# Kernel optimization log

Measured on AMD Instinct MI355X. Metric: run time of the kernel, lower is better.

## Reference

```python
import jax, jax.numpy as jnp
import numpy as np

EPS_NORM = 1e-6
EPS_MM = 1e-5


def feature_l2norm(f, axis=1):
    # torch: f / sqrt(sum(f^2, dim) + 1e-6)
    return f / jnp.sqrt(jnp.sum(f * f, axis=axis, keepdims=True) + EPS_NORM)


def mutual_matching(c):
    # c: [b, 1, f1, f2, f3, f4]
    b, ch, f1, f2, f3, f4 = c.shape
    # max over (f1,f2) for each (f3,f4) target location
    max_B = jnp.max(c.reshape(b, f1 * f2, f3, f4), axis=1).reshape(b, 1, 1, 1, f3, f4)
    # max over (f3,f4) for each (f1,f2) source location
    max_A = jnp.max(c.reshape(b, f1 * f2, f3 * f4), axis=2).reshape(b, 1, f1, f2, 1, 1)
    return c * (c / (max_A + EPS_MM)) * (c / (max_B + EPS_MM))


def correlation4d(fa, fb):
    # fa: [b,c,hA,wA], fb: [b,c,hB,wB] -> [b,1,hA,wA,hB,wB]
    corr = jnp.einsum('bcij,bckl->bijkl', fa, fb)[:, None]
    corr = jax.nn.relu(corr)
    return feature_l2norm(corr, axis=1)  # channel dim is 1 -> x/sqrt(x^2+eps)


def conv4d(x, w, b):
    # x: [B,Ci,f1,f2,f3,f4]; w: [Co,Ci,k,k,k,k]; b: [Co]
    # Implemented as a sum of k 3D convs over (f2,f3,f4), sliding along f1 --
    # exactly the Conv4d emulation used by NC-Net.
    B, Ci, f1, f2, f3, f4 = x.shape
    Co, _, k = w.shape[:3]
    p = k // 2
    xp = jnp.pad(x, ((0, 0), (0, 0), (p, p), (0, 0), (0, 0), (0, 0)))
    out = None
    for i in range(k):
        xi = jax.lax.dynamic_slice_in_dim(xp, i, f1, axis=2)        # [B,Ci,f1,f2,f3,f4]
        xi = xi.transpose(0, 2, 1, 3, 4, 5).reshape(B * f1, Ci, f2, f3, f4)
        yi = jax.lax.conv_general_dilated(
            xi, w[:, :, i], window_strides=(1, 1, 1),
            padding=[(p, p)] * 3,
            dimension_numbers=('NCDHW', 'OIDHW', 'NCDHW'))
        yi = yi.reshape(B, f1, Co, f2, f3, f4).transpose(0, 2, 1, 3, 4, 5)
        out = yi if out is None else out + yi
    return out + b[None, :, None, None, None, None]


def nc_stack(x, params):
    # Sequential(Conv4d, ReLU) x 3
    for w, b in params:
        x = jax.nn.relu(conv4d(x, w, b))
    return x


def neigh_consensus(x, params):
    # symmetric mode: conv(x) + conv(x.permute(0,1,4,5,2,3)).permute back
    ya = nc_stack(x, params)
    yb = nc_stack(x.transpose(0, 1, 4, 5, 2, 3), params).transpose(0, 1, 4, 5, 2, 3)
    return ya + yb


def setup_inputs() -> dict:
    key = jax.random.key(0)
    ks = jax.random.split(key, 8)
    b, c, h, w = 4, 256, 32, 32
    feature_A = jax.random.normal(ks[0], (b, c, h, w), dtype=jnp.float32)
    feature_B = jax.random.normal(ks[1], (b, c, h, w), dtype=jnp.float32)
    k = 3
    w1 = jax.random.normal(ks[2], (10, 1, k, k, k, k), dtype=jnp.float32) * 0.05
    b1 = jnp.zeros((10,), jnp.float32)
    w2 = jax.random.normal(ks[3], (10, 10, k, k, k, k), dtype=jnp.float32) * 0.05
    b2 = jnp.zeros((10,), jnp.float32)
    w3 = jax.random.normal(ks[4], (1, 10, k, k, k, k), dtype=jnp.float32) * 0.05
    b3 = jnp.zeros((1,), jnp.float32)
    return {"feature_A": feature_A, "feature_B": feature_B,
            "w1": w1, "b1": b1, "w2": w2, "b2": b2, "w3": w3, "b3": b3}


def reference(feature_A, feature_B, w1, b1, w2, b2, w3, b3):
    fa = feature_l2norm(feature_A, axis=1)
    fb = feature_l2norm(feature_B, axis=1)
    corr4d = correlation4d(fa, fb)                   # [b,1,hA,wA,hB,wB]
    corr4d = mutual_matching(corr4d)
    corr4d = neigh_consensus(corr4d, [(w1, b1), (w2, b2), (w3, b3)])
    corr4d = mutual_matching(corr4d)
    return corr4d
```

## Files before the change

kernel.cpp:

```cpp
#include <hip/hip_runtime.h>

#define EPSN 1e-6f
#define EPSM 1e-5f

typedef __fp16 h2v __attribute__((ext_vector_type(2)));

__device__ __forceinline__ unsigned pkh2(float a, float b) {
    union { h2v h; unsigned u; } v;
    v.h = __builtin_amdgcn_cvt_pkrtz(a, b);
    return v.u;
}

__device__ __forceinline__ float dot2f(unsigned a, unsigned b, float c) {
    union { unsigned u; h2v h; } ua, ub;
    ua.u = a; ub.u = b;
#if __has_builtin(__builtin_amdgcn_fdot2)
    return __builtin_amdgcn_fdot2(ua.h, ub.h, c, false);
#else
    return fmaf((float)ua.h.x, (float)ub.h.x,
                fmaf((float)ua.h.y, (float)ub.h.y, c));
#endif
}

__global__ __launch_bounds__(256) void invnorm_k(const float* __restrict__ f,
                                                 float* __restrict__ inv)
{
    int pbase = blockIdx.x * 64;
    int pp = threadIdx.x & 63;
    int cc = threadIdx.x >> 6;
    int pos = pbase + pp;
    int b = pos >> 10, ij = pos & 1023;
    const float* fp = f + (size_t)(b * 256) * 1024 + ij;
    float s = 0.f;
    #pragma unroll 8
    for (int k = 0; k < 64; ++k) {
        float v = fp[(size_t)(cc * 64 + k) * 1024];
        s += v * v;
    }
    __shared__ float red[4][64];
    red[cc][pp] = s;
    __syncthreads();
    if (cc == 0) {
        float t = red[0][pp] + red[1][pp] + red[2][pp] + red[3][pp];
        inv[pos] = rsqrtf(t + EPSN);
    }
}

__global__ __launch_bounds__(256) void corr_k(const float* __restrict__ fa,
                                              const float* __restrict__ fb,
                                              const float* __restrict__ invA,
                                              const float* __restrict__ invB,
                                              float* __restrict__ corr)
{
    __shared__ float As[16][68];
    __shared__ float Bs[16][68];
    int b = blockIdx.z;
    int i0 = blockIdx.y * 64, j0 = blockIdx.x * 64;
    int tid = threadIdx.x;
    int tx = tid & 15, ty = tid >> 4;
    const float* fab = fa + (size_t)b * 256 * 1024;
    const float* fbb = fb + (size_t)b * 256 * 1024;
    const float* ia = invA + b * 1024 + i0;
    const float* ib = invB + b * 1024 + j0;
    float acc[4][4] = {};
    for (int kc = 0; kc < 256; kc += 16) {
        #pragma unroll
        for (int l = 0; l < 4; ++l) {
            int idx = tid + l * 256;
            int r = idx >> 6, cix = idx & 63;
            As[r][cix] = fab[(size_t)(kc + r) * 1024 + i0 + cix] * ia[cix];
            Bs[r][cix] = fbb[(size_t)(kc + r) * 1024 + j0 + cix] * ib[cix];
        }
        __syncthreads();
        #pragma unroll
        for (int k = 0; k < 16; ++k) {
            float4 av = *(const float4*)&As[k][ty * 4];
            float4 bv = *(const float4*)&Bs[k][tx * 4];
            float a[4] = {av.x, av.y, av.z, av.w};
            float bq[4] = {bv.x, bv.y, bv.z, bv.w};
            #pragma unroll
            for (int ii = 0; ii < 4; ++ii)
                #pragma unroll
                for (int jj = 0; jj < 4; ++jj)
                    acc[ii][jj] += a[ii] * bq[jj];
        }
        __syncthreads();
    }
    float* cb = corr + ((size_t)b << 20);
    #pragma unroll
    for (int ii = 0; ii < 4; ++ii) {
        float4 o; float v;
        v = fmaxf(acc[ii][0], 0.f); o.x = v * rsqrtf(v * v + EPSN);
        v = fmaxf(acc[ii][1], 0.f); o.y = v * rsqrtf(v * v + EPSN);
        v = fmaxf(acc[ii][2], 0.f); o.z = v * rsqrtf(v * v + EPSN);
        v = fmaxf(acc[ii][3], 0.f); o.w = v * rsqrtf(v * v + EPSN);
        *(float4*)&cb[(size_t)(i0 + ty * 4 + ii) * 1024 + j0 + tx * 4] = o;
    }
}

__global__ __launch_bounds__(256) void rowmax_k(const float* __restrict__ c,
                                                float* __restrict__ maxR)
{
    int b = blockIdx.y, i = blockIdx.x, tid = threadIdx.x;
    const float* row = c + ((size_t)b << 20) + ((size_t)i << 10);
    float m = fmaxf(fmaxf(row[tid], row[tid + 256]), fmaxf(row[tid + 512], row[tid + 768]));
    #pragma unroll
    for (int off = 32; off; off >>= 1) m = fmaxf(m, __shfl_down(m, off, 64));
    __shared__ float sred[4];
    if ((tid & 63) == 0) sred[tid >> 6] = m;
    __syncthreads();
    if (tid == 0)
        maxR[b * 1024 + i] = fmaxf(fmaxf(sred[0], sred[1]), fmaxf(sred[2], sred[3]));
}

__global__ __launch_bounds__(256) void colmax_k(const float* __restrict__ c,
                                                float* __restrict__ maxC)
{
    int j = blockIdx.x * 256 + threadIdx.x;
    int r0 = blockIdx.y * 128;
    int b = blockIdx.z;
    const float* cb = c + ((size_t)b << 20);
    float m = 0.f;
    for (int r = 0; r < 128; ++r) m = fmaxf(m, cb[(size_t)(r0 + r) * 1024 + j]);
    atomicMax((int*)&maxC[b * 1024 + j], __float_as_int(m));
}

__global__ __launch_bounds__(256) void mmapply_k(float* __restrict__ c,
                                                 const float* __restrict__ maxR,
                                                 const float* __restrict__ maxC)
{
    int e4 = blockIdx.x * 256 + threadIdx.x;
    int e = e4 * 4;
    int b = e >> 20, i = (e >> 10) & 1023, j0 = e & 1023;
    float4 v = ((float4*)c)[e4];
    float ra = 1.f / (maxR[b * 1024 + i] + EPSM);
    float4 mb = ((const float4*)maxC)[(b * 1024 + j0) >> 2];
    float4 o;
    o.x = v.x * v.x * v.x * ra / (mb.x + EPSM);
    o.y = v.y * v.y * v.y * ra / (mb.y + EPSM);
    o.z = v.z * v.z * v.z * ra / (mb.z + EPSM);
    o.w = v.w * v.w * v.w * ra / (mb.w + EPSM);
    ((float4*)c)[e4] = o;
}

template <int CI, int CO>
__global__ void packw_k(const float* __restrict__ w, float* __restrict__ dst, int perm)
{
    constexpr int WS = (3 * CO + 3) & ~3;
    int idx = blockIdx.x * 256 + threadIdx.x;
    if (idx >= CI * 27 * WS) return;
    int ci = idx / (27 * WS);
    int rem = idx - ci * 27 * WS;
    int d123 = rem / WS;
    int slot = rem - d123 * WS;
    float v = 0.f;
    if (slot < 3 * CO) {
        int d4 = slot / CO, co = slot - d4 * CO;
        int t = d123 * 3 + d4;
        int d1 = t / 27, r2 = t % 27;
        int d2 = r2 / 9, r3 = r2 % 9;
        int d3 = r3 / 3, dd4 = r3 % 3;
        int st = perm ? (d3 * 27 + dd4 * 9 + d1 * 3 + d2) : t;
        v = w[(co * CI + ci) * 81 + st];
    }
    dst[idx] = v;
}

template <int CIP, int CO>
__global__ void packw2_k(const float* __restrict__ w, unsigned* __restrict__ dst, int perm)
{
    constexpr int WS = (3 * CO + 3) & ~3;
    int idx = blockIdx.x * 256 + threadIdx.x;
    if (idx >= CIP * 27 * WS) return;
    int pp = idx / (27 * WS);
    int rem = idx - pp * 27 * WS;
    int d123 = rem / WS;
    int slot = rem - d123 * WS;
    unsigned v = 0u;
    if (slot < 3 * CO) {
        int d4 = slot / CO, co = slot - d4 * CO;
        int t = d123 * 3 + d4;
        int d1 = t / 27, r2 = t % 27;
        int d2 = r2 / 9, r3 = r2 % 9;
        int d3 = r3 / 3, dd4 = r3 % 3;
        int st = perm ? (d3 * 27 + dd4 * 9 + d1 * 3 + d2) : t;
        float f0 = w[(co * 2 * CIP + 2 * pp) * 81 + st];
        float f1 = w[(co * 2 * CIP + 2 * pp + 1) * 81 + st];
        v = pkh2(f0, f1);
    }
    dst[idx] = v;
}

template <int CI, int CO, bool ADD>
__global__ __launch_bounds__(256, 4) void conv4d_k(const float* __restrict__ x,
                                                   const float* __restrict__ wp,
                                                   const float* __restrict__ bias,
                                                   float* __restrict__ y)
{
    constexpr int WS = (3 * CO + 3) & ~3;
    constexpr int NW4 = WS / 4;
    constexpr int SLAB = 34 * 35;
    __shared__ float tile[3 * SLAB];

    int tid = threadIdx.x;
    int f1 = blockIdx.x >> 5, f2 = blockIdx.x & 31;
    int q = tid & 7, yy = tid >> 3;
    int x0 = q << 2;

    for (int e = tid; e < 3 * SLAB; e += 256) tile[e] = 0.f;

    float acc[CO][4];
    #pragma unroll
    for (int co = 0; co < CO; ++co) {
        float bv = bias[co];
        acc[co][0] = bv; acc[co][1] = bv; acc[co][2] = bv; acc[co][3] = bv;
    }

    float bufA[WS], bufB[WS];

#define TAP(U, WB, WN, PF) do {                                               \
        constexpr int u_ = (U);                                               \
        const float* rowb_ = &tile[(u_/3)*SLAB + (yy + u_%3)*35 + x0];        \
        float xs_[6];                                                         \
        _Pragma("unroll") for (int j = 0; j < 6; ++j) xs_[j] = rowb_[j];      \
        if (PF) {                                                             \
            _Pragma("unroll") for (int k = 0; k < NW4; ++k)                   \
                *(float4*)&WN[k*4] =                                          \
                    ((const float4*)(wphase + (u_+1)*WS))[k];                 \
        }                                                                     \
        _Pragma("unroll") for (int d4 = 0; d4 < 3; ++d4)                      \
        _Pragma("unroll") for (int co = 0; co < CO; ++co) {                   \
            float wf_ = WB[d4*CO + co];                                       \
            _Pragma("unroll") for (int p = 0; p < 4; ++p)                     \
                acc[co][p] = fmaf(xs_[p + d4], wf_, acc[co][p]);              \
        }                                                                     \
    } while (0)

    #pragma unroll 1
    for (int ci = 0; ci < CI; ++ci) {
        const float* wci = wp + ci * 27 * WS;
        #pragma unroll 1
        for (int d1 = 0; d1 < 3; ++d1) {
            int g1 = f1 + d1 - 1;
            bool g1ok = (unsigned)g1 < 32u;
            const float* wphase = wci + d1 * 9 * WS;
            __syncthreads();
            #pragma unroll
            for (int k = 0; k < NW4; ++k)
                *(float4*)&bufA[k*4] = ((const float4*)wphase)[k];
            #pragma unroll
            for (int it = 0; it < 3; ++it) {
                int e = tid + it * 256;
                int s2 = e >> 8, rr = (e >> 3) & 31, qq = e & 7;
                int g2 = f2 + s2 - 1;
                float4 v = {0.f, 0.f, 0.f, 0.f};
                if (g1ok & ((unsigned)g2 < 32u))
                    v = *(const float4*)&x[((size_t)ci << 20) +
                        ((size_t)((g1 << 5) + g2) << 10) + (rr << 5) + (qq << 2)];
                float* t = &tile[s2 * SLAB + (rr + 1) * 35 + 1 + (qq << 2)];
                t[0] = v.x; t[1] = v.y; t[2] = v.z; t[3] = v.w;
            }
            __syncthreads();

            TAP(0, bufA, bufB, true);
            TAP(1, bufB, bufA, true);
            TAP(2, bufA, bufB, true);
            TAP(3, bufB, bufA, true);
            TAP(4, bufA, bufB, true);
            TAP(5, bufB, bufA, true);
            TAP(6, bufA, bufB, true);
            TAP(7, bufB, bufA, true);
            TAP(8, bufA, bufB, false);
        }
    }
#undef TAP

    size_t obase = ((size_t)(f1 * 32 + f2) << 10) + yy * 32 + x0;
    #pragma unroll
    for (int co = 0; co < CO; ++co) {
        float4 o;
        o.x = fmaxf(acc[co][0], 0.f);
        o.y = fmaxf(acc[co][1], 0.f);
        o.z = fmaxf(acc[co][2], 0.f);
        o.w = fmaxf(acc[co][3], 0.f);
        float* yp = y + ((size_t)co << 20) + obase;
        if (ADD) {
            float4 prev = *(const float4*)yp;
            o.x += prev.x; o.y += prev.y; o.z += prev.z; o.w += prev.w;
        }
        *(float4*)yp = o;
    }
}

template <int CIP, int CO, bool ADD>
__global__ __launch_bounds__(256, 4) void conv4dp_k(const float* __restrict__ x,
                                                    const unsigned* __restrict__ wp,
                                                    const float* __restrict__ bias,
                                                    float* __restrict__ y)
{
    constexpr int WS = (3 * CO + 3) & ~3;
    constexpr int NW4 = WS / 4;
    constexpr int SLAB = 34 * 35;
    __shared__ unsigned tile[3 * SLAB];

    int tid = threadIdx.x;
    int f1 = blockIdx.x >> 5, f2 = blockIdx.x & 31;
    int q = tid & 7, yy = tid >> 3;
    int x0 = q << 2;

    for (int e = tid; e < 3 * SLAB; e += 256) tile[e] = 0u;

    float acc[CO][4];
    #pragma unroll
    for (int co = 0; co < CO; ++co) {
        float bv = bias[co];
        acc[co][0] = bv; acc[co][1] = bv; acc[co][2] = bv; acc[co][3] = bv;
    }

    unsigned bufA[WS], bufB[WS];

#define TAPP(U, WB, WN, PF) do {                                              \
        constexpr int u_ = (U);                                               \
        const unsigned* rowb_ = &tile[(u_/3)*SLAB + (yy + u_%3)*35 + x0];     \
        unsigned xs_[6];                                                      \
        _Pragma("unroll") for (int j = 0; j < 6; ++j) xs_[j] = rowb_[j];      \
        if (PF) {                                                             \
            _Pragma("unroll") for (int k = 0; k < NW4; ++k)                   \
                *(uint4*)&WN[k*4] =                                           \
                    ((const uint4*)(wphase + (u_+1)*WS))[k];                  \
        }                                                                     \
        _Pragma("unroll") for (int d4 = 0; d4 < 3; ++d4)                      \
        _Pragma("unroll") for (int co = 0; co < CO; ++co) {                   \
            unsigned wf_ = WB[d4*CO + co];                                    \
            _Pragma("unroll") for (int p = 0; p < 4; ++p)                     \
                acc[co][p] = dot2f(xs_[p + d4], wf_, acc[co][p]);             \
        }                                                                     \
    } while (0)

    #pragma unroll 1
    for (int pp = 0; pp < CIP; ++pp) {
        const float* xc0 = x + ((size_t)(2 * pp) << 20);
        const float* xc1 = x + ((size_t)(2 * pp + 1) << 20);
        const unsigned* wci = wp + pp * 27 * WS;
        #pragma unroll 1
        for (int d1 = 0; d1 < 3; ++d1) {
            int g1 = f1 + d1 - 1;
            bool g1ok = (unsigned)g1 < 32u;
            const unsigned* wphase = wci + d1 * 9 * WS;
            __syncthreads();
            #pragma unroll
            for (int k = 0; k < NW4; ++k)
                *(uint4*)&bufA[k*4] = ((const uint4*)wphase)[k];
            #pragma unroll
            for (int it = 0; it < 3; ++it) {
                int e = tid + it * 256;
                int s2 = e >> 8, rr = (e >> 3) & 31, qq = e & 7;
                int g2 = f2 + s2 - 1;
                float4 va = {0.f, 0.f, 0.f, 0.f};
                float4 vb = {0.f, 0.f, 0.f, 0.f};
                if (g1ok & ((unsigned)g2 < 32u)) {
                    size_t off = ((size_t)((g1 << 5) + g2) << 10) + (rr << 5) + (qq << 2);
                    va = *(const float4*)&xc0[off];
                    vb = *(const float4*)&xc1[off];
                }
                unsigned* t = &tile[s2 * SLAB + (rr + 1) * 35 + 1 + (qq << 2)];
                t[0] = pkh2(va.x, vb.x);
                t[1] = pkh2(va.y, vb.y);
                t[2] = pkh2(va.z, vb.z);
                t[3] = pkh2(va.w, vb.w);
            }
            __syncthreads();

            TAPP(0, bufA, bufB, true);
            TAPP(1, bufB, bufA, true);
            TAPP(2, bufA, bufB, true);
            TAPP(3, bufB, bufA, true);
            TAPP(4, bufA, bufB, true);
            TAPP(5, bufB, bufA, true);
            TAPP(6, bufA, bufB, true);
            TAPP(7, bufB, bufA, true);
            TAPP(8, bufA, bufB, false);
        }
    }
#undef TAPP

    size_t obase = ((size_t)(f1 * 32 + f2) << 10) + yy * 32 + x0;
    #pragma unroll
    for (int co = 0; co < CO; ++co) {
        float4 o;
        o.x = fmaxf(acc[co][0], 0.f);
        o.y = fmaxf(acc[co][1], 0.f);
        o.z = fmaxf(acc[co][2], 0.f);
        o.w = fmaxf(acc[co][3], 0.f);
        float* yp = y + ((size_t)co << 20) + obase;
        if (ADD) {
            float4 prev = *(const float4*)yp;
            o.x += prev.x; o.y += prev.y; o.z += prev.z; o.w += prev.w;
        }
        *(float4*)yp = o;
    }
}

extern "C" void kernel_launch(void* const* d_in, const int* in_sizes, int n_in,
                              void* d_out, int out_size, void* d_ws, size_t ws_size,
                              hipStream_t stream)
{
    (void)in_sizes; (void)n_in; (void)out_size; (void)ws_size;
    const float* fA = (const float*)d_in[0];
    const float* fB = (const float*)d_in[1];
    const float* w1 = (const float*)d_in[2];
    const float* b1 = (const float*)d_in[3];
    const float* w2 = (const float*)d_in[4];
    const float* b2 = (const float*)d_in[5];
    const float* w3 = (const float*)d_in[6];
    const float* b3 = (const float*)d_in[7];
    float* out = (float*)d_out;
    float* ws = (float*)d_ws;

    size_t o = 0;
    float* invA = ws + o; o += 4096;
    float* invB = ws + o; o += 4096;
    float* maxR = ws + o; o += 4096;
    float* maxC = ws + o; o += 4096;
    float* pw1  = ws + o; o += 2048;
    unsigned* pw2 = (unsigned*)(ws + o); o += 8640;
    unsigned* pw3 = (unsigned*)(ws + o); o += 1080;
    float* corr = ws + o; o += 4194304;
    float* t1   = ws + o; o += 10485760;
    float* t2   = ws + o; o += 10485760;

    invnorm_k<<<64, 256, 0, stream>>>(fA, invA);
    invnorm_k<<<64, 256, 0, stream>>>(fB, invB);
    corr_k<<<dim3(16, 16, 4), 256, 0, stream>>>(fA, fB, invA, invB, corr);

    rowmax_k<<<dim3(1024, 4), 256, 0, stream>>>(corr, maxR);
    (void)hipMemsetAsync(maxC, 0, 4096 * sizeof(float), stream);
    colmax_k<<<dim3(4, 8, 4), 256, 0, stream>>>(corr, maxC);
    mmapply_k<<<4096, 256, 0, stream>>>(corr, maxR, maxC);

    packw_k<1, 10><<<4, 256, 0, stream>>>(w1, pw1, 0);
    packw_k<1, 10><<<4, 256, 0, stream>>>(w1, pw1 + 864, 1);
    packw2_k<5, 10><<<17, 256, 0, stream>>>(w2, pw2, 0);
    packw2_k<5, 10><<<17, 256, 0, stream>>>(w2, pw2 + 4320, 1);
    packw2_k<5, 1><<<3, 256, 0, stream>>>(w3, pw3, 0);
    packw2_k<5, 1><<<3, 256, 0, stream>>>(w3, pw3 + 540, 1);

    for (int b = 0; b < 4; ++b) {
        const float* xb = corr + (size_t)b * 1048576;
        float* ob = out + (size_t)b * 1048576;
        conv4d_k<1, 10, false><<<1024, 256, 0, stream>>>(xb, pw1, b1, t1);
        conv4dp_k<5, 10, false><<<1024, 256, 0, stream>>>(t1, pw2, b2, t2);
        conv4dp_k<5, 1, false><<<1024, 256, 0, stream>>>(t2, pw3, b3, ob);
        conv4d_k<1, 10, false><<<1024, 256, 0, stream>>>(xb, pw1 + 864, b1, t1);
        conv4dp_k<5, 10, false><<<1024, 256, 0, stream>>>(t1, pw2 + 4320, b2, t2);
        conv4dp_k<5, 1, true ><<<1024, 256, 0, stream>>>(t2, pw3 + 540, b3, ob);
    }

    rowmax_k<<<dim3(1024, 4), 256, 0, stream>>>(out, maxR);
    (void)hipMemsetAsync(maxC, 0, 4096 * sizeof(float), stream);
    colmax_k<<<dim3(4, 8, 4), 256, 0, stream>>>(out, maxC);
    mmapply_k<<<4096, 256, 0, stream>>>(out, maxR, maxC);
}
```

Before: 1.829 ms.

## Use MFMA f16 for middle 10-to-10 conv4d and store intermediates as packed half

Replaces the middle 10x10-channel conv4d, previously done with packed fdot2 in VALU, with a new kernel that runs 16x16x16 f16 MFMA instructions over the 81 taps, keeping the input channels padded to 16 in a shared-memory tile. The first and middle layers now write their outputs as packed fp16 channel pairs, which halves intermediate memory traffic and lets later layers skip the float-to-half conversion on load. The cost is padding waste (10 of 16 channels used), many small scalar global loads when filling the tile, and additional fp16 rounding of the intermediate activations.

Result: faster. 1.659 ms (-9.3%).

```diff
diff --git a/kernel.cpp b/kernel.cpp
--- a/kernel.cpp
+++ b/kernel.cpp
@@ -4,6 +4,10 @@
 #define EPSM 1e-5f
 
 typedef __fp16 h2v __attribute__((ext_vector_type(2)));
+typedef __fp16 f16x4 __attribute__((ext_vector_type(4)));
+typedef float f32x4 __attribute__((ext_vector_type(4)));
+
+#define MFMA16(a, b, c) __builtin_amdgcn_mfma_f32_16x16x16f16((a), (b), (c), 0, 0, 0)
 
 __device__ __forceinline__ unsigned pkh2(float a, float b) {
     union { h2v h; unsigned u; } v;
@@ -164,6 +168,27 @@
         v = w[(co * CI + ci) * 81 + st];
     }
     dst[idx] = v;
+}
+
+__global__ void packwm_k(const float* __restrict__ w, unsigned short* __restrict__ dst,
+                         int perm)
+{
+    int idx = blockIdx.x * 256 + threadIdx.x;
+    if (idx >= 20736) return;
+    int tap = idx >> 8;
+    int co  = (idx >> 4) & 15;
+    int k   = idx & 15;
+    float v = 0.f;
+    if (co < 10 && k < 10) {
+        int d1 = tap / 27, r2 = tap % 27;
+        int d2 = r2 / 9, r3 = r2 % 9;
+        int d3 = r3 / 3, d4 = r3 % 3;
+        int st = perm ? (d3 * 27 + d4 * 9 + d1 * 3 + d2) : tap;
+        v = w[(co * 10 + k) * 81 + st];
+    }
+    union { __fp16 h; unsigned short u; } cv;
+    cv.h = (__fp16)v;
+    dst[idx] = cv.u;
 }
 
 template <int CIP, int CO>
@@ -191,7 +216,7 @@
     dst[idx] = v;
 }
 
-template <int CI, int CO, bool ADD>
+template <int CI, int CO, bool ADD, bool PACK>
 __global__ __launch_bounds__(256, 4) void conv4d_k(const float* __restrict__ x,
                                                    const float* __restrict__ wp,
                                                    const float* __restrict__ bias,
@@ -276,24 +301,146 @@
 #undef TAP
 
     size_t obase = ((size_t)(f1 * 32 + f2) << 10) + yy * 32 + x0;
+    if (PACK) {
+        unsigned* ypu = (unsigned*)y;
+        #pragma unroll
+        for (int c = 0; c < CO / 2; ++c) {
+            uint4 o;
+            o.x = pkh2(fmaxf(acc[2*c][0], 0.f), fmaxf(acc[2*c+1][0], 0.f));
+            o.y = pkh2(fmaxf(acc[2*c][1], 0.f), fmaxf(acc[2*c+1][1], 0.f));
+            o.z = pkh2(fmaxf(acc[2*c][2], 0.f), fmaxf(acc[2*c+1][2], 0.f));
+            o.w = pkh2(fmaxf(acc[2*c][3], 0.f), fmaxf(acc[2*c+1][3], 0.f));
+            *(uint4*)&ypu[(size_t)c * 1048576 + obase] = o;
+        }
+    } else {
+        #pragma unroll
+        for (int co = 0; co < CO; ++co) {
+            float4 o;
+            o.x = fmaxf(acc[co][0], 0.f);
+            o.y = fmaxf(acc[co][1], 0.f);
+            o.z = fmaxf(acc[co][2], 0.f);
+            o.w = fmaxf(acc[co][3], 0.f);
+            float* yp = y + ((size_t)co << 20) + obase;
+            if (ADD) {
+                float4 prev = *(const float4*)yp;
+                o.x += prev.x; o.y += prev.y; o.z += prev.z; o.w += prev.w;
+            }
+            *(float4*)yp = o;
+        }
+    }
+}
+
+__global__ __launch_bounds__(256, 4) void conv4dm_k(const unsigned* __restrict__ xp,
+                                                    const unsigned short* __restrict__ wm,
+                                                    const float* __restrict__ bias,
+                                                    unsigned* __restrict__ yp)
+{
+    __shared__ unsigned tile[3 * 10 * 34 * 9];
+
+    int tid = threadIdx.x;
+    int bx = blockIdx.x;
+    int q  = bx & 3;
+    int f2 = (bx >> 2) & 31;
+    int f1 = bx >> 7;
+    int l  = tid & 63;
+    int wv = tid >> 6;
+    int sl = l & 15;
+    int g  = l >> 4;
+
+    for (int e = tid; e < 9180; e += 256) tile[e] = 0u;
+
+    f32x4 bv;
     #pragma unroll
-    for (int co = 0; co < CO; ++co) {
-        float4 o;
-        o.x = fmaxf(acc[co][0], 0.f);
-        o.y = fmaxf(acc[co][1], 0.f);
-        o.z = fmaxf(acc[co][2], 0.f);
-        o.w = fmaxf(acc[co][3], 0.f);
-        float* yp = y + ((size_t)co << 20) + obase;
-        if (ADD) {
-            float4 prev = *(const float4*)yp;
-            o.x += prev.x; o.y += prev.y; o.z += prev.z; o.w += prev.w;
-        }
-        *(float4*)yp = o;
-    }
+    for (int e = 0; e < 4; ++e) {
+        int co = 4 * g + e;
+        bv[e] = (co < 10) ? bias[co] : 0.f;
+    }
+    f32x4 acc0 = bv, acc1 = bv, acc2 = bv, acc3 = bv;
+
+    int qbase = q * 8;
+
+    #pragma unroll 1
+    for (int d1 = 0; d1 < 3; ++d1) {
+        int g1 = f1 + d1 - 1;
+        bool g1ok = (unsigned)g1 < 32u;
+        __syncthreads();
+
+        uint2 aw[27];
+        #pragma unroll
+        for (int t27 = 0; t27 < 27; ++t27) {
+            int tap = d1 * 27 + t27;
+            aw[t27] = *(const uint2*)&wm[(tap << 8) + (sl << 4) + (g << 2)];
+        }
+
+        #pragma unroll
+        for (int it = 0; it < 4; ++it) {
+            int e = tid + it * 256;
+            if (e < 960) {
+                int c  = (e & 31) + 1;
+                int rg = e >> 5;
+                int r  = rg % 10;
+                int s2 = rg / 10;
+                int g2 = f2 + s2 - 1;
+                int g3 = qbase + r - 1;
+                unsigned v0 = 0, v1 = 0, v2 = 0, v3 = 0, v4 = 0;
+                if (g1ok & ((unsigned)g2 < 32u) & ((unsigned)g3 < 32u)) {
+                    size_t off = ((size_t)((g1 << 5) + g2) << 10) + (g3 << 5) + (c - 1);
+                    v0 = xp[off];
+                    v1 = xp[off + 1048576];
+                    v2 = xp[off + 2097152];
+                    v3 = xp[off + 3145728];
+                    v4 = xp[off + 4194304];
+                }
+                unsigned* t = &tile[((s2 * 10 + r) * 34 + c) * 9];
+                t[0] = v0; t[1] = v1; t[2] = v2; t[3] = v3; t[4] = v4;
+            }
+        }
+        __syncthreads();
+
+        int tb0 = ((wv * 2 + 0) * 34 + sl) * 9 + (g << 1);
+        #pragma unroll
+        for (int d2 = 0; d2 < 3; ++d2)
+        #pragma unroll
+        for (int d3 = 0; d3 < 3; ++d3)
+        #pragma unroll
+        for (int d4 = 0; d4 < 3; ++d4) {
+            int t27 = d2 * 9 + d3 * 3 + d4;
+            union { uint2 u; f16x4 h; } A; A.u = aw[t27];
+            int tapoff = ((d2 * 10 + d3) * 34 + d4) * 9;
+            const unsigned* bp = &tile[tb0 + tapoff];
+            union { uint2 u; f16x4 h; } B;
+            B.u.x = bp[0];           B.u.y = bp[1];
+            acc0 = MFMA16(A.h, B.h, acc0);
+            B.u.x = bp[16 * 9];      B.u.y = bp[16 * 9 + 1];
+            acc1 = MFMA16(A.h, B.h, acc1);
+            B.u.x = bp[34 * 9];      B.u.y = bp[34 * 9 + 1];
+            acc2 = MFMA16(A.h, B.h, acc2);
+            B.u.x = bp[50 * 9];      B.u.y = bp[50 * 9 + 1];
+            acc3 = MFMA16(A.h, B.h, acc3);
+        }
+    }
+
+    size_t pbase = ((size_t)((f1 << 5) + f2) << 10);
+#define STORE_TILE(ACC, RT, CH) do {                                          \
+        size_t sidx = pbase + ((size_t)(qbase + (RT)) << 5) + (CH) * 16 + sl; \
+        float r0 = fmaxf((ACC)[0], 0.f), r1 = fmaxf((ACC)[1], 0.f);           \
+        float r2 = fmaxf((ACC)[2], 0.f), r3 = fmaxf((ACC)[3], 0.f);           \
+        if (g < 2) {                                                          \
+            yp[(size_t)(2 * g)     * 1048576 + sidx] = pkh2(r0, r1);          \
+            yp[(size_t)(2 * g + 1) * 1048576 + sidx] = pkh2(r2, r3);          \
+        } else if (g == 2) {                                                  \
+            yp[(size_t)4 * 1048576 + sidx] = pkh2(r0, r1);                    \
+        }                                                                     \
+    } while (0)
+    STORE_TILE(acc0, wv * 2 + 0, 0);
+    STORE_TILE(acc1, wv * 2 + 0, 1);
+    STORE_TILE(acc2, wv * 2 + 1, 0);
+    STORE_TILE(acc3, wv * 2 + 1, 1);
+#undef STORE_TILE
 }
 
 template <int CIP, int CO, bool ADD>
-__global__ __launch_bounds__(256, 4) void conv4dp_k(const float* __restrict__ x,
+__global__ __launch_bounds__(256, 4) void conv4dp_k(const unsigned* __restrict__ xp,
                                                     const unsigned* __restrict__ wp,
                                                     const float* __restrict__ bias,
                                                     float* __restrict__ y)
@@ -313,8 +460,8 @@
     float acc[CO][4];
     #pragma unroll
     for (int co = 0; co < CO; ++co) {
-        float bv = bias[co];
-        acc[co][0] = bv; acc[co][1] = bv; acc[co][2] = bv; acc[co][3] = bv;
+        float bvv = bias[co];
+        acc[co][0] = bvv; acc[co][1] = bvv; acc[co][2] = bvv; acc[co][3] = bvv;
     }
 
     unsigned bufA[WS], bufB[WS];
@@ -339,8 +486,6 @@
 
     #pragma unroll 1
     for (int pp = 0; pp < CIP; ++pp) {
-        const float* xc0 = x + ((size_t)(2 * pp) << 20);
-        const float* xc1 = x + ((size_t)(2 * pp + 1) << 20);
         const unsigned* wci = wp + pp * 27 * WS;
         #pragma unroll 1
         for (int d1 = 0; d1 < 3; ++d1) {
@@ -356,18 +501,12 @@
                 int e = tid + it * 256;
                 int s2 = e >> 8, rr = (e >> 3) & 31, qq = e & 7;
                 int g2 = f2 + s2 - 1;
-                float4 va = {0.f, 0.f, 0.f, 0.f};
-                float4 vb = {0.f, 0.f, 0.f, 0.f};
-                if (g1ok & ((unsigned)g2 < 32u)) {
-                    size_t off = ((size_t)((g1 << 5) + g2) << 10) + (rr << 5) + (qq << 2);
-                    va = *(const float4*)&xc0[off];
-                    vb = *(const float4*)&xc1[off];
-                }
+                uint4 v = {0u, 0u, 0u, 0u};
+                if (g1ok & ((unsigned)g2 < 32u))
+                    v = *(const uint4*)&xp[((size_t)pp << 20) +
+                        ((size_t)((g1 << 5) + g2) << 10) + (rr << 5) + (qq << 2)];
                 unsigned* t = &tile[s2 * SLAB + (rr + 1) * 35 + 1 + (qq << 2)];
-                t[0] = pkh2(va.x, vb.x);
-                t[1] = pkh2(va.y, vb.y);
-                t[2] = pkh2(va.z, vb.z);
-                t[3] = pkh2(va.w, vb.w);
+                t[0] = v.x; t[1] = v.y; t[2] = v.z; t[3] = v.w;
             }
             __syncthreads();
 
@@ -392,12 +531,12 @@
         o.y = fmaxf(acc[co][1], 0.f);
         o.z = fmaxf(acc[co][2], 0.f);
         o.w = fmaxf(acc[co][3], 0.f);
-        float* yp = y + ((size_t)co << 20) + obase;
+        float* ypt = y + ((size_t)co << 20) + obase;
         if (ADD) {
-            float4 prev = *(const float4*)yp;
+            float4 prev = *(const float4*)ypt;
             o.x += prev.x; o.y += prev.y; o.z += prev.z; o.w += prev.w;
         }
-        *(float4*)yp = o;
+        *(float4*)ypt = o;
     }
 }
 
@@ -423,11 +562,11 @@
     float* maxR = ws + o; o += 4096;
     float* maxC = ws + o; o += 4096;
     float* pw1  = ws + o; o += 2048;
-    unsigned* pw2 = (unsigned*)(ws + o); o += 8640;
+    unsigned short* wm2 = (unsigned short*)(ws + o); o += 20736;
     unsigned* pw3 = (unsigned*)(ws + o); o += 1080;
     float* corr = ws + o; o += 4194304;
-    float* t1   = ws + o; o += 10485760;
-    float* t2   = ws + o; o += 10485760;
+    unsigned* t1p = (unsigned*)(ws + o); o += 5242880;
+    unsigned* t2p = (unsigned*)(ws + o); o += 5242880;
 
     invnorm_k<<<64, 256, 0, stream>>>(fA, invA);
     invnorm_k<<<64, 256, 0, stream>>>(fB, invB);
@@ -440,20 +579,20 @@
 
     packw_k<1, 10><<<4, 256, 0, stream>>>(w1, pw1, 0);
     packw_k<1, 10><<<4, 256, 0, stream>>>(w1, pw1 + 864, 1);
-    packw2_k<5, 10><<<17, 256, 0, stream>>>(w2, pw2, 0);
-    packw2_k<5, 10><<<17, 256, 0, stream>>>(w2, pw2 + 4320, 1);
+    packwm_k<<<81, 256, 0, stream>>>(w2, wm2, 0);
+    packwm_k<<<81, 256, 0, stream>>>(w2, wm2 + 20736, 1);
     packw2_k<5, 1><<<3, 256, 0, stream>>>(w3, pw3, 0);
     packw2_k<5, 1><<<3, 256, 0, stream>>>(w3, pw3 + 540, 1);
 
     for (int b = 0; b < 4; ++b) {
         const float* xb = corr + (size_t)b * 1048576;
         float* ob = out + (size_t)b * 1048576;
-        conv4d_k<1, 10, false><<<1024, 256, 0, stream>>>(xb, pw1, b1, t1);
-        conv4dp_k<5, 10, false><<<1024, 256, 0, stream>>>(t1, pw2, b2, t2);
-        conv4dp_k<5, 1, false><<<1024, 256, 0, stream>>>(t2, pw3, b3, ob);
-        conv4d_k<1, 10, false><<<1024, 256, 0, stream>>>(xb, pw1 + 864, b1, t1);
-        conv4dp_k<5, 10, false><<<1024, 256, 0, stream>>>(t1, pw2 + 4320, b2, t2);
-        conv4dp_k<5, 1, true ><<<1024, 256, 0, stream>>>(t2, pw3 + 540, b3, ob);
+        conv4d_k<1, 10, false, true><<<1024, 256, 0, stream>>>(xb, pw1, b1, (float*)t1p);
+        conv4dm_k<<<4096, 256, 0, stream>>>(t1p, wm2, b2, t2p);
+        conv4dp_k<5, 1, false><<<1024, 256, 0, stream>>>(t2p, pw3, b3, ob);
+        conv4d_k<1, 10, false, true><<<1024, 256, 0, stream>>>(xb, pw1 + 864, b1, (float*)t1p);
+        conv4dm_k<<<4096, 256, 0, stream>>>(t1p, wm2 + 20736, b2, t2p);
+        conv4dp_k<5, 1, true ><<<1024, 256, 0, stream>>>(t2p, pw3 + 540, b3, ob);
     }
 
     rowmax_k<<<dim3(1024, 4), 256, 0, stream>>>(out, maxR);
```
